# Optimization experiments

Measured on AMD Instinct MI355X. Metric: run time of the kernel, lower is better.

The kernel has to match this reference:

```python
import jax, jax.numpy as jnp
import numpy as np

D_MODEL = 1024
H = 16
D_K = D_MODEL // H  # 64
B, S = 2, 2048


def setup_inputs() -> dict:
    key = jax.random.key(0)
    ks = jax.random.split(key, 8)
    scale = 1.0 / np.sqrt(D_MODEL)
    return {
        "q": jax.random.normal(ks[0], (B, S, D_MODEL), dtype=jnp.float32),
        "k": jax.random.normal(ks[1], (B, S, D_MODEL), dtype=jnp.float32),
        "v": jax.random.normal(ks[2], (B, S, D_MODEL), dtype=jnp.float32),
        "W_q": jax.random.normal(ks[3], (H, D_MODEL, D_K), dtype=jnp.float32) * scale,
        "W_k": jax.random.normal(ks[4], (H, D_MODEL, D_K), dtype=jnp.float32) * scale,
        "W_v": jax.random.normal(ks[5], (H, D_MODEL, D_K), dtype=jnp.float32) * scale,
        "W_o": jax.random.normal(ks[6], (D_MODEL, H * D_K), dtype=jnp.float32) * scale,
        "b_o": jnp.zeros((D_MODEL,), dtype=jnp.float32),
    }


def reference(q, k, v, W_q, W_k, W_v, W_o, b_o):
    b, s, _ = q.shape
    h, _, d_k = W_q.shape
    inv_sqrt_dk = jnp.asarray(1.0 / np.sqrt(d_k), q.dtype)
    # per-head projections: [b, h, s, d_k]
    qh = jnp.einsum("bsd,hdk->bhsk", q, W_q)
    kh = jnp.einsum("bsd,hdk->bhsk", k, W_k)
    vh = jnp.einsum("bsd,hdk->bhsk", v, W_v)
    # scaled dot product attention
    scores = jnp.einsum("bhqk,bhsk->bhqs", qh, kh) * inv_sqrt_dk  # [b,h,S,S]
    attn = jax.nn.softmax(scores, axis=-1)
    ctx = jnp.einsum("bhqs,bhsk->bhqk", attn, vh)  # [b,h,S,d_k]
    # chunk over heads + concat along feature dim -> [b, S, h*d_k], head-major
    ctx = ctx.transpose(0, 2, 1, 3).reshape(b, s, h * d_k)
    # final linear
    return ctx @ W_o.T + b_o
```

## Files before the change

kernel.cpp:

```cpp
#include <hip/hip_runtime.h>
#include <cstdint>
#include <cstddef>


typedef unsigned short bf16_t;
typedef __attribute__((ext_vector_type(8))) short short8;
typedef __attribute__((ext_vector_type(4))) float f32x4;

__device__ __forceinline__ uint32_t fbits(float f) {
  union { float f; uint32_t u; } v; v.f = f; return v.u;
}
__device__ __forceinline__ bf16_t f2bf(float f) {
  uint32_t u = fbits(f);
  return (bf16_t)((u + 0x7FFFu + ((u >> 16) & 1u)) >> 16);
}
__device__ __forceinline__ uint32_t packbf2(float lo, float hi) {
  uint32_t a = fbits(hi) + 0x8000u;
  uint32_t b = fbits(lo) + 0x8000u;
  return __builtin_amdgcn_perm(a, b, 0x07060302u);
}
__device__ __forceinline__ int4 cvt8(f32x4 lo, f32x4 hi) {
  return make_int4((int)packbf2(lo.x, lo.y), (int)packbf2(lo.z, lo.w),
                   (int)packbf2(hi.x, hi.y), (int)packbf2(hi.z, hi.w));
}

__device__ __forceinline__ void gload16(const bf16_t* g, bf16_t* l) {
  __builtin_amdgcn_global_load_lds(
      (const __attribute__((address_space(1))) void*)g,
      (__attribute__((address_space(3))) void*)l, 16, 0, 0);
}

__global__ void prep_kernel(const float* __restrict__ Wo,
                            const float* __restrict__ Wq, const float* __restrict__ Wk,
                            const float* __restrict__ Wv,
                            const float* __restrict__ q, const float* __restrict__ k,
                            const float* __restrict__ v,
                            bf16_t* __restrict__ Woo,
                            bf16_t* __restrict__ Wtq, bf16_t* __restrict__ Wtk,
                            bf16_t* __restrict__ Wtv,
                            bf16_t* __restrict__ qb, bf16_t* __restrict__ kb,
                            bf16_t* __restrict__ vb) {
  int blk = blockIdx.x;
  int tid = threadIdx.x;
  if (blk < 1024) {
    int i = blk * 256 + tid;
    f32x4 val = ((const f32x4*)Wo)[i];
    ushort4 o;
    o.x = f2bf(val.x); o.y = f2bf(val.y); o.z = f2bf(val.z); o.w = f2bf(val.w);
    ((ushort4*)Woo)[i] = o;
  } else if (blk < 2560) {
    int blk2 = blk - 1024;
    int z = blk2 >> 9, t = blk2 & 511;
    const float* W = z == 0 ? Wq : z == 1 ? Wk : Wv;
    bf16_t* Wt = z == 0 ? Wtq : z == 1 ? Wtk : Wtv;
    int h = t >> 5, d0 = (t & 31) * 32;
    __shared__ float tile[32][65];
    const float* src = W + ((size_t)h << 16) + (size_t)d0 * 64;
    int d = tid >> 3;
#pragma unroll
    for (int j = 0; j < 2; j++) {
      int dk = (tid & 7) * 8 + j * 4;
      *(f32x4*)&tile[d][dk] = *(const f32x4*)(src + d * 64 + dk);
    }
    __syncthreads();
    int dk2 = tid >> 2, c = tid & 3;
    union { ushort s[8]; int4 v; } o;
#pragma unroll
    for (int j = 0; j < 8; j++) o.s[j] = f2bf(tile[c * 8 + j][dk2]);
    *(int4*)(Wt + (size_t)(h * 64 + dk2) * 1024 + d0 + c * 8) = o.v;
  } else {
    int blk3 = blk - 2560;
    int z = blk3 >> 11;
    int t3 = blk3 & 2047;
    const float* src = z == 0 ? q : z == 1 ? k : v;
    bf16_t* dst = z == 0 ? qb : z == 1 ? kb : vb;
    int i = t3 * 256 + tid;
    f32x4 lo = ((const f32x4*)src)[i * 2];
    f32x4 hi = ((const f32x4*)src)[i * 2 + 1];
    ((int4*)dst)[i] = cvt8(lo, hi);
  }
}

__global__ __launch_bounds__(256) void gemm_proj_kernel(
    const bf16_t* __restrict__ A0, const bf16_t* __restrict__ A1, const bf16_t* __restrict__ A2,
    const bf16_t* __restrict__ B0, const bf16_t* __restrict__ B1, const bf16_t* __restrict__ B2,
    bf16_t* __restrict__ O0, bf16_t* __restrict__ O1, bf16_t* __restrict__ O2,
    float s0)
{
  const int bid = blockIdx.x;
  const int nIdx = bid / 96;
  const int g = bid - nIdx * 96;
  const int z = g % 3;
  const int m0 = (g / 3) * 128, n0 = nIdx * 128;

  const bf16_t* A  = z == 0 ? A0 : z == 1 ? A1 : A2;
  const bf16_t* Bt = z == 0 ? B0 : z == 1 ? B1 : B2;
  bf16_t* Cout     = z == 0 ? O0 : z == 1 ? O1 : O2;
  const float scale = z == 0 ? s0 : 1.0f;
  const int K = 1024;

  __shared__ alignas(16) bf16_t smem[18432];

  const int tid = threadIdx.x;
  const int lane = tid & 63, wave = tid >> 6;
  const int wm = wave >> 1, wn = wave & 1;
  const int quad = lane >> 4, l15 = lane & 15;

  f32x4 acc[4][4];
#pragma unroll
  for (int i = 0; i < 4; i++)
#pragma unroll
    for (int j = 0; j < 4; j++) acc[i][j] = (f32x4)0.0f;

  const int srow = tid >> 2, scol = (tid & 3) * 8;
  const bf16_t* pa0 = A  + (size_t)(m0 + srow) * K + scol;
  const bf16_t* pa1 = pa0 + (size_t)64 * K;
  const bf16_t* pb0 = Bt + (size_t)(n0 + srow) * K + scol;
  const bf16_t* pb1 = pb0 + (size_t)64 * K;
  const int lws = wave * 512;

  gload16(pa0, smem + lws);
  gload16(pa1, smem + 2048 + lws);
  gload16(pb0, smem + 4096 + lws);
  gload16(pb1, smem + 6144 + lws);
  __syncthreads();

  for (int it = 0; it < 32; ++it) {
    const int cur = (it & 1) * 8192;
    if (it < 31) {
      const int nxt = ((it + 1) & 1) * 8192;
      const int ko = (it + 1) * 32;
      gload16(pa0 + ko, smem + nxt + lws);
      gload16(pa1 + ko, smem + nxt + 2048 + lws);
      gload16(pb0 + ko, smem + nxt + 4096 + lws);
      gload16(pb1 + ko, smem + nxt + 6144 + lws);
    }

    short8 af[4], bfr[4];
#pragma unroll
    for (int mi = 0; mi < 4; mi++)
      af[mi] = *(const short8*)(smem + cur + (wm * 64 + mi * 16 + l15) * 32 + quad * 8);
#pragma unroll
    for (int ni = 0; ni < 4; ni++)
      bfr[ni] = *(const short8*)(smem + cur + 4096 + (wn * 64 + ni * 16 + l15) * 32 + quad * 8);
#pragma unroll
    for (int mi = 0; mi < 4; mi++)
#pragma unroll
      for (int ni = 0; ni < 4; ni++)
        acc[mi][ni] = __builtin_amdgcn_mfma_f32_16x16x32_bf16(af[mi], bfr[ni], acc[mi][ni], 0, 0, 0);

    __syncthreads();
  }

  const int s0r = m0 & 2047, bb = m0 >> 11, hp = n0 >> 6;
  if (z < 2) {
    bf16_t* slot = smem + wn * 9216;
#pragma unroll
    for (int ni = 0; ni < 4; ni++)
#pragma unroll
      for (int mi = 0; mi < 4; mi++)
#pragma unroll
        for (int r = 0; r < 4; r++)
          slot[(wm * 64 + mi * 16 + quad * 4 + r) * 72 + ni * 16 + l15] =
              f2bf(acc[mi][ni][r] * scale);
    __syncthreads();
#pragma unroll
    for (int rd = 0; rd < 8; ++rd) {
      int idx = rd * 256 + tid;
      int si = idx >> 10, mm = (idx >> 3) & 127, c8 = idx & 7;
      int4 val = *(const int4*)(smem + si * 9216 + mm * 72 + c8 * 8);
      *(int4*)(Cout + ((size_t)((bb * 16 + hp + si) * 2048 + s0r + mm)) * 64 + c8 * 8) = val;
    }
  } else {
    bf16_t* slot = smem + wn * 8704;
#pragma unroll
    for (int ni = 0; ni < 4; ni++)
#pragma unroll
      for (int mi = 0; mi < 4; mi++) {
        uint2 pk = make_uint2(packbf2(acc[mi][ni][0], acc[mi][ni][1]),
                              packbf2(acc[mi][ni][2], acc[mi][ni][3]));
        *(uint2*)(slot + (ni * 16 + l15) * 136 + wm * 64 + mi * 16 + quad * 4) = pk;
      }
    __syncthreads();
#pragma unroll
    for (int rd = 0; rd < 8; ++rd) {
      int idx = rd * 256 + tid;
      int si = idx >> 10, c = (idx >> 4) & 63, ck = idx & 15;
      int4 val = *(const int4*)(smem + si * 8704 + c * 136 + ck * 8);
      *(int4*)(Cout + (size_t)(bb * 16 + hp + si) * 131072 + (size_t)c * 2048 + s0r + ck * 8) = val;
    }
  }
}

__global__ __launch_bounds__(256) void gemm_out_kernel(
    const bf16_t* __restrict__ A, const bf16_t* __restrict__ Bt,
    float* __restrict__ C, const float* __restrict__ bias)
{
  const int K = 1024, N = 1024;
  __shared__ alignas(16) bf16_t smem[12288];
  const int tid = threadIdx.x;
  const int lane = tid & 63, wave = tid >> 6;
  const int quad = lane >> 4, l15 = lane & 15;
  const int m0 = (blockIdx.x & 31) * 128, n0 = (blockIdx.x >> 5) * 64;

  f32x4 acc[2][4];
#pragma unroll
  for (int i = 0; i < 2; i++)
#pragma unroll
    for (int j = 0; j < 4; j++) acc[i][j] = (f32x4)0.0f;

  const int srow = tid >> 2, scol = (tid & 3) * 8;
  const bf16_t* pa0 = A  + (size_t)(m0 + srow) * K + scol;
  const bf16_t* pa1 = pa0 + (size_t)64 * K;
  const bf16_t* pb  = Bt + (size_t)(n0 + srow) * K + scol;
  const int lws = wave * 512;

  gload16(pa0, smem + lws);
  gload16(pa1, smem + 2048 + lws);
  gload16(pb,  smem + 4096 + lws);
  __syncthreads();

  for (int it = 0; it < 32; ++it) {
    const int cur = (it & 1) * 6144;
    if (it < 31) {
      const int nxt = ((it + 1) & 1) * 6144;
      const int ko = (it + 1) * 32;
      gload16(pa0 + ko, smem + nxt + lws);
      gload16(pa1 + ko, smem + nxt + 2048 + lws);
      gload16(pb + ko,  smem + nxt + 4096 + lws);
    }

    short8 af[2], bfr[4];
#pragma unroll
    for (int mi = 0; mi < 2; mi++)
      af[mi] = *(const short8*)(smem + cur + (wave * 32 + mi * 16 + l15) * 32 + quad * 8);
#pragma unroll
    for (int ni = 0; ni < 4; ni++)
      bfr[ni] = *(const short8*)(smem + cur + 4096 + (ni * 16 + l15) * 32 + quad * 8);
#pragma unroll
    for (int mi = 0; mi < 2; mi++)
#pragma unroll
      for (int ni = 0; ni < 4; ni++)
        acc[mi][ni] = __builtin_amdgcn_mfma_f32_16x16x32_bf16(af[mi], bfr[ni], acc[mi][ni], 0, 0, 0);

    __syncthreads();
  }

#pragma unroll
  for (int ni = 0; ni < 4; ni++) {
    int col = n0 + ni * 16 + l15;
    float bv = bias[col];
#pragma unroll
    for (int mi = 0; mi < 2; mi++) {
      int row = m0 + wave * 32 + mi * 16 + quad * 4;
#pragma unroll
      for (int r = 0; r < 4; r++)
        C[(size_t)(row + r) * N + col] = acc[mi][ni][r] + bv;
    }
  }
}

__global__ __launch_bounds__(512) void flash_kernel(
    const bf16_t* __restrict__ qh, const bf16_t* __restrict__ kh,
    const bf16_t* __restrict__ vT, bf16_t* __restrict__ ctx)
{
  __shared__ alignas(16) bf16_t KtF[2][4096];
  __shared__ alignas(16) bf16_t VtF[2][4096];
  __shared__ alignas(16) bf16_t PtF[16384];
  const int tid = threadIdx.x, lane = tid & 63, wave = tid >> 6;
  const int quad = lane >> 4, l15 = lane & 15;
  const int gid = blockIdx.x;
  const int hb = gid & 31;
  const int h = hb & 15, b = hb >> 4;
  const int q0 = (gid >> 5) * 256;
  const size_t headoff = (size_t)hb * 2048 * 64;
  const bf16_t* Q = qh + headoff;
  const bf16_t* K = kh + headoff;
  const bf16_t* V = vT + headoff;

  short8 qf[2][2];
#pragma unroll
  for (int g = 0; g < 2; g++)
#pragma unroll
    for (int ks = 0; ks < 2; ks++)
      qf[g][ks] = *(const short8*)(Q + (size_t)(q0 + wave * 32 + g * 16 + l15) * 64
                                   + ks * 32 + quad * 8);

  f32x4 O[2][4];
#pragma unroll
  for (int g = 0; g < 2; g++)
#pragma unroll
    for (int mi = 0; mi < 4; mi++) O[g][mi] = (f32x4)0.0f;
  f32x4 lacc[2] = {(f32x4)0.0f, (f32x4)0.0f};

  const bf16_t* Kp = K + (size_t)((wave >> 1) * 16 + l15) * 64 + (wave & 1) * 32 + quad * 8;
  const bf16_t* Vp = V + (size_t)((wave >> 1) * 16 + l15) * 2048 + (wave & 1) * 32 + quad * 8;
  const int soff = wave * 512 + lane * 8;
  const int pwb = wave * 4096 + ((quad >> 1) * 16 + l15) * 16 + 8 * (quad & 1);

  auto body = [&](int buf) {
    f32x4 S[2][4];
#pragma unroll
    for (int g = 0; g < 2; g++)
#pragma unroll
      for (int mi = 0; mi < 4; mi++) S[g][mi] = (f32x4)0.0f;
#pragma unroll
    for (int ks = 0; ks < 2; ks++) {
#pragma unroll
      for (int mi = 0; mi < 4; mi++) {
        short8 kf = *(const short8*)(&KtF[buf][(mi * 2 + ks) * 512 + lane * 8]);
        S[0][mi] = __builtin_amdgcn_mfma_f32_16x16x32_bf16(kf, qf[0][ks], S[0][mi], 0, 0, 0);
        S[1][mi] = __builtin_amdgcn_mfma_f32_16x16x32_bf16(kf, qf[1][ks], S[1][mi], 0, 0, 0);
      }
    }
#pragma unroll
    for (int g = 0; g < 2; g++) {
#pragma unroll
      for (int mi = 0; mi < 4; mi++)
#pragma unroll
        for (int r = 0; r < 4; r++)
          S[g][mi][r] = __builtin_amdgcn_exp2f(S[g][mi][r]);
      lacc[g] += (S[g][0] + S[g][1]) + (S[g][2] + S[g][3]);
    }
#pragma unroll
    for (int g = 0; g < 2; g++)
#pragma unroll
      for (int mi = 0; mi < 4; mi++) {
        uint2 pk = make_uint2(packbf2(S[g][mi][0], S[g][mi][1]),
                              packbf2(S[g][mi][2], S[g][mi][3]));
        *(uint2*)((char*)PtF + pwb + g * 2048 + (mi >> 1) * 1024 + (mi & 1) * 512) = pk;
      }
#pragma unroll
    for (int ks = 0; ks < 2; ks++) {
      short8 pf0 = *(const short8*)(&PtF[wave * 2048 + (ks * 64 + lane) * 8]);
      short8 pf1 = *(const short8*)(&PtF[wave * 2048 + 1024 + (ks * 64 + lane) * 8]);
#pragma unroll
      for (int mi = 0; mi < 4; mi++) {
        short8 vf = *(const short8*)(&VtF[buf][(mi * 2 + ks) * 512 + lane * 8]);
        O[0][mi] = __builtin_amdgcn_mfma_f32_16x16x32_bf16(vf, pf0, O[0][mi], 0, 0, 0);
        O[1][mi] = __builtin_amdgcn_mfma_f32_16x16x32_bf16(vf, pf1, O[1][mi], 0, 0, 0);
      }
    }
  };

  int4 k0 = *(const int4*)Kp, v0 = *(const int4*)Vp;
  *(int4*)(&KtF[0][soff]) = k0;
  *(int4*)(&VtF[0][soff]) = v0;
  int4 kA = *(const int4*)(Kp + 4096), vA = *(const int4*)(Vp + 64);
  __syncthreads();

  for (int it = 0; it < 32; it += 2) {
    *(int4*)(&KtF[1][soff]) = kA;
    *(int4*)(&VtF[1][soff]) = vA;
    int4 kB, vB;
    if (it + 2 < 32) {
      kB = *(const int4*)(Kp + (size_t)(it + 2) * 4096);
      vB = *(const int4*)(Vp + (size_t)(it + 2) * 64);
    }
    body(0);
    __syncthreads();

    if (it + 2 < 32) {
      *(int4*)(&KtF[0][soff]) = kB;
      *(int4*)(&VtF[0][soff]) = vB;
    }
    if (it + 3 < 32) {
      kA = *(const int4*)(Kp + (size_t)(it + 3) * 4096);
      vA = *(const int4*)(Vp + (size_t)(it + 3) * 64);
    }
    body(1);
    __syncthreads();
  }

#pragma unroll
  for (int g = 0; g < 2; g++) {
    float l = (lacc[g][0] + lacc[g][1]) + (lacc[g][2] + lacc[g][3]);
    l += __shfl_xor(l, 16, 64);
    l += __shfl_xor(l, 32, 64);
    float inv = 1.0f / l;
    int qrow = q0 + wave * 32 + g * 16 + l15;
    bf16_t* crow = ctx + ((size_t)(b * 2048 + qrow)) * 1024 + h * 64;
#pragma unroll
    for (int mi = 0; mi < 4; mi++) {
      uint2 pk = make_uint2(packbf2(O[g][mi][0] * inv, O[g][mi][1] * inv),
                            packbf2(O[g][mi][2] * inv, O[g][mi][3] * inv));
      *(uint2*)(crow + mi * 16 + quad * 4) = pk;
    }
  }
}

extern "C" void kernel_launch(void* const* d_in, const int* in_sizes, int n_in,
                              void* d_out, int out_size, void* d_ws, size_t ws_size,
                              hipStream_t stream)
{
  const float* q  = (const float*)d_in[0];
  const float* k  = (const float*)d_in[1];
  const float* v  = (const float*)d_in[2];
  const float* Wq = (const float*)d_in[3];
  const float* Wk = (const float*)d_in[4];
  const float* Wv = (const float*)d_in[5];
  const float* Wo = (const float*)d_in[6];
  const float* bo = (const float*)d_in[7];
  float* out = (float*)d_out;

  const size_t NX = (size_t)4096 * 1024;
  const size_t NW = (size_t)1024 * 1024;

  char* p = (char*)d_ws;
  bf16_t* Wtq = (bf16_t*)p; p += NW * 2;
  bf16_t* Wtk = (bf16_t*)p; p += NW * 2;
  bf16_t* Wtv = (bf16_t*)p; p += NW * 2;
  bf16_t* Wob = (bf16_t*)p; p += NW * 2;
  bf16_t* qb  = (bf16_t*)p; p += NX * 2;
  bf16_t* kb  = (bf16_t*)p; p += NX * 2;
  bf16_t* vb  = (bf16_t*)p; p += NX * 2;
  bf16_t* qhb = (bf16_t*)p; p += NX * 2;
  bf16_t* khb = (bf16_t*)p; p += NX * 2;
  bf16_t* vTb = (bf16_t*)p; p += NX * 2;
  bf16_t* ctxb = (bf16_t*)p; p += NX * 2;

  prep_kernel<<<8704, 256, 0, stream>>>(Wo, Wq, Wk, Wv, q, k, v,
                                        Wob, Wtq, Wtk, Wtv, qb, kb, vb);

  const float qscale = 0.125f * 1.44269504088896340736f;
  gemm_proj_kernel<<<768, 256, 0, stream>>>(qb, kb, vb, Wtq, Wtk, Wtv,
                                            qhb, khb, vTb, qscale);

  flash_kernel<<<256, 512, 0, stream>>>(qhb, khb, vTb, ctxb);

  gemm_out_kernel<<<512, 256, 0, stream>>>(ctxb, Wob, out, bo);

  (void)in_sizes; (void)n_in; (void)out_size; (void)ws_size;
}
```

Before: 208.8 us.

## Split flash attention into 512 blocks of 256 threads with 128-query tiles

The flash kernel now runs 4 waves per block over 128 query rows instead of 8 waves over 256, so there are twice as many blocks to spread across the CUs. Each thread loads two K/V chunks per tile, keeping the same tile-loading plan with fewer threads. Shared memory for P is halved. The trade-off is that each block re-reads the K/V stream for fewer queries, which doubles total K/V traffic, in exchange for more even filling of the CUs.

```diff
diff --git a/kernel.cpp b/kernel.cpp
--- a/kernel.cpp
+++ b/kernel.cpp
@@ -260,19 +260,19 @@
   }
 }
 
-__global__ __launch_bounds__(512) void flash_kernel(
+__global__ __launch_bounds__(256) void flash_kernel(
     const bf16_t* __restrict__ qh, const bf16_t* __restrict__ kh,
     const bf16_t* __restrict__ vT, bf16_t* __restrict__ ctx)
 {
   __shared__ alignas(16) bf16_t KtF[2][4096];
   __shared__ alignas(16) bf16_t VtF[2][4096];
-  __shared__ alignas(16) bf16_t PtF[16384];
+  __shared__ alignas(16) bf16_t PtF[8192];
   const int tid = threadIdx.x, lane = tid & 63, wave = tid >> 6;
   const int quad = lane >> 4, l15 = lane & 15;
   const int gid = blockIdx.x;
   const int hb = gid & 31;
   const int h = hb & 15, b = hb >> 4;
-  const int q0 = (gid >> 5) * 256;
+  const int q0 = (gid >> 5) * 128;
   const size_t headoff = (size_t)hb * 2048 * 64;
   const bf16_t* Q = qh + headoff;
   const bf16_t* K = kh + headoff;
@@ -343,30 +343,38 @@
     }
   };
 
-  int4 k0 = *(const int4*)Kp, v0 = *(const int4*)Vp;
-  *(int4*)(&KtF[0][soff]) = k0;
-  *(int4*)(&VtF[0][soff]) = v0;
-  int4 kA = *(const int4*)(Kp + 4096), vA = *(const int4*)(Vp + 64);
+  {
+    int4 k0a = *(const int4*)Kp,           v0a = *(const int4*)Vp;
+    int4 k0b = *(const int4*)(Kp + 2048),  v0b = *(const int4*)(Vp + 65536);
+    *(int4*)(&KtF[0][soff]) = k0a;         *(int4*)(&VtF[0][soff]) = v0a;
+    *(int4*)(&KtF[0][soff + 2048]) = k0b;  *(int4*)(&VtF[0][soff + 2048]) = v0b;
+  }
+  int4 kAa = *(const int4*)(Kp + 4096),         vAa = *(const int4*)(Vp + 64);
+  int4 kAb = *(const int4*)(Kp + 4096 + 2048),  vAb = *(const int4*)(Vp + 64 + 65536);
   __syncthreads();
 
   for (int it = 0; it < 32; it += 2) {
-    *(int4*)(&KtF[1][soff]) = kA;
-    *(int4*)(&VtF[1][soff]) = vA;
-    int4 kB, vB;
+    *(int4*)(&KtF[1][soff]) = kAa;         *(int4*)(&VtF[1][soff]) = vAa;
+    *(int4*)(&KtF[1][soff + 2048]) = kAb;  *(int4*)(&VtF[1][soff + 2048]) = vAb;
+    int4 kBa, kBb, vBa, vBb;
     if (it + 2 < 32) {
-      kB = *(const int4*)(Kp + (size_t)(it + 2) * 4096);
-      vB = *(const int4*)(Vp + (size_t)(it + 2) * 64);
+      kBa = *(const int4*)(Kp + (size_t)(it + 2) * 4096);
+      kBb = *(const int4*)(Kp + (size_t)(it + 2) * 4096 + 2048);
+      vBa = *(const int4*)(Vp + (size_t)(it + 2) * 64);
+      vBb = *(const int4*)(Vp + (size_t)(it + 2) * 64 + 65536);
     }
     body(0);
     __syncthreads();
 
     if (it + 2 < 32) {
-      *(int4*)(&KtF[0][soff]) = kB;
-      *(int4*)(&VtF[0][soff]) = vB;
+      *(int4*)(&KtF[0][soff]) = kBa;         *(int4*)(&VtF[0][soff]) = vBa;
+      *(int4*)(&KtF[0][soff + 2048]) = kBb;  *(int4*)(&VtF[0][soff + 2048]) = vBb;
     }
     if (it + 3 < 32) {
-      kA = *(const int4*)(Kp + (size_t)(it + 3) * 4096);
-      vA = *(const int4*)(Vp + (size_t)(it + 3) * 64);
+      kAa = *(const int4*)(Kp + (size_t)(it + 3) * 4096);
+      kAb = *(const int4*)(Kp + (size_t)(it + 3) * 4096 + 2048);
+      vAa = *(const int4*)(Vp + (size_t)(it + 3) * 64);
+      vAb = *(const int4*)(Vp + (size_t)(it + 3) * 64 + 65536);
     }
     body(1);
     __syncthreads();
@@ -426,7 +434,7 @@
   gemm_proj_kernel<<<768, 256, 0, stream>>>(qb, kb, vb, Wtq, Wtk, Wtv,
                                             qhb, khb, vTb, qscale);
 
-  flash_kernel<<<256, 512, 0, stream>>>(qhb, khb, vTb, ctxb);
+  flash_kernel<<<512, 256, 0, stream>>>(qhb, khb, vTb, ctxb);
 
   gemm_out_kernel<<<512, 256, 0, stream>>>(ctxb, Wob, out, bo);
 
```

Result: no change. 208.5 us (-0.1%).
